# Performance work log

Measured on AMD Instinct MI355X. Metric: run time of the kernel, lower is better.

## Reference

```python
import jax, jax.numpy as jnp
import numpy as np

EMBED = 1024
HEADS = 16
HEAD_DIM = EMBED // HEADS
FF = 4 * EMBED
B, S = 2, 2048


def setup_inputs() -> dict:
    key = jax.random.key(0)
    ks = jax.random.split(key, 16)
    sd = 0.02
    inp = {
        "x": jax.random.normal(ks[0], (B, S, EMBED), dtype=jnp.float32),
        "Wq": jax.random.normal(ks[1], (EMBED, EMBED), dtype=jnp.float32) * sd,
        "bq": jnp.zeros((EMBED,), jnp.float32),
        "Wk": jax.random.normal(ks[2], (EMBED, EMBED), dtype=jnp.float32) * sd,
        "bk": jnp.zeros((EMBED,), jnp.float32),
        "Wv": jax.random.normal(ks[3], (EMBED, EMBED), dtype=jnp.float32) * sd,
        "bv": jnp.zeros((EMBED,), jnp.float32),
        "Wo": jax.random.normal(ks[4], (EMBED, EMBED), dtype=jnp.float32) * sd,
        "W1": jax.random.normal(ks[5], (EMBED, FF), dtype=jnp.float32) * sd,
        "b1": jnp.zeros((FF,), jnp.float32),
        "W2": jax.random.normal(ks[6], (FF, EMBED), dtype=jnp.float32) * sd,
        "b2": jnp.zeros((EMBED,), jnp.float32),
        "g1": jnp.ones((EMBED,), jnp.float32),
        "be1": jnp.zeros((EMBED,), jnp.float32),
        "g2": jnp.ones((EMBED,), jnp.float32),
        "be2": jnp.zeros((EMBED,), jnp.float32),
    }
    return inp


def _layernorm(x, g, b, eps=1e-5):
    mu = jnp.mean(x, axis=-1, keepdims=True)
    var = jnp.mean(jnp.square(x - mu), axis=-1, keepdims=True)
    return (x - mu) * jax.lax.rsqrt(var + eps) * g + b


def _attn(x, Wq, bq, Wk, bk, Wv, bv, Wo):
    b, s, d = x.shape
    q = (x @ Wq + bq).reshape(b, s, HEADS, HEAD_DIM)
    k = (x @ Wk + bk).reshape(b, s, HEADS, HEAD_DIM)
    v = (x @ Wv + bv).reshape(b, s, HEADS, HEAD_DIM)
    # NOTE: original scales by sqrt(embed_dim), NOT sqrt(head_dim)
    logits = jnp.einsum('bqhd,bkhd->bhqk', q, k) / jnp.sqrt(jnp.float32(d))
    mask = jnp.tril(jnp.ones((s, s), dtype=bool))
    logits = jnp.where(mask, logits, -jnp.inf)
    w = jax.nn.softmax(logits, axis=-1)
    z = jnp.einsum('bhqk,bkhd->bqhd', w, v).reshape(b, s, d)
    return z @ Wo


def reference(x, Wq, bq, Wk, bk, Wv, bv, Wo, W1, b1, W2, b2, g1, be1, g2, be2):
    h = x + _attn(_layernorm(x, g1, be1), Wq, bq, Wk, bk, Wv, bv, Wo)
    m = _layernorm(h, g2, be2)
    m = jax.nn.gelu(m @ W1 + b1, approximate=False) @ W2 + b2
    return h + m
```

## Files before the change

kernel.cpp:

```cpp
#include <hip/hip_runtime.h>
#include <cstdint>
#include <cstddef>
#include <math.h>

#define EMBED 1024
#define SEQ   2048
#define NROWS 4096
#define NHEADS 16

typedef __bf16 bf16x8 __attribute__((ext_vector_type(8)));
typedef float f32x4 __attribute__((ext_vector_type(4)));
typedef unsigned short us8 __attribute__((ext_vector_type(8)));
typedef unsigned short us4 __attribute__((ext_vector_type(4)));

__device__ __forceinline__ unsigned short f2bf(float f) {
  union { float f; unsigned u; } v; v.f = f;
  unsigned r = v.u + 0x7fffu + ((v.u >> 16) & 1u);
  return (unsigned short)(r >> 16);
}
__device__ __forceinline__ float bf2f(unsigned short u) {
  union { unsigned u; float f; } v; v.u = (unsigned)u << 16; return v.f;
}

__device__ __forceinline__ bf16x8 as_bf(us8 u) { return __builtin_bit_cast(bf16x8, u); }

__device__ __forceinline__ void gload_lds16(const unsigned short* g, unsigned short* l) {
  __builtin_amdgcn_global_load_lds((const __attribute__((address_space(1))) void*)g,
                                   (__attribute__((address_space(3))) void*)l, 16, 0, 0);
}

__global__ __launch_bounds__(256) void transpose_to_bf16(
    const float* __restrict__ in, unsigned short* __restrict__ out, int K, int N) {
  __shared__ float tile[32][33];
  const int tx = threadIdx.x & 31, ty = threadIdx.x >> 5;
  const int n0 = blockIdx.x * 32, k0 = blockIdx.y * 32;
#pragma unroll
  for (int i = 0; i < 4; i++) {
    int k = ty + i * 8;
    tile[k][tx] = in[(size_t)(k0 + k) * N + n0 + tx];
  }
  __syncthreads();
#pragma unroll
  for (int i = 0; i < 4; i++) {
    int n = ty + i * 8;
    out[(size_t)(n0 + n) * K + k0 + tx] = f2bf(tile[tx][n]);
  }
}

__global__ __launch_bounds__(256) void layernorm_bf16(
    const float* __restrict__ x, const float* __restrict__ g,
    const float* __restrict__ be, unsigned short* __restrict__ out) {
  const int wave = threadIdx.x >> 6, lane = threadIdx.x & 63;
  const int row = blockIdx.x * 4 + wave;
  const float* xr = x + (size_t)row * EMBED;
  float4 v[4];
  float s = 0.f, sq = 0.f;
#pragma unroll
  for (int c = 0; c < 4; c++) {
    v[c] = *(const float4*)&xr[c * 256 + lane * 4];
    s  += v[c].x + v[c].y + v[c].z + v[c].w;
    sq += v[c].x * v[c].x + v[c].y * v[c].y + v[c].z * v[c].z + v[c].w * v[c].w;
  }
#pragma unroll
  for (int m = 1; m < 64; m <<= 1) {
    s  += __shfl_xor(s, m, 64);
    sq += __shfl_xor(sq, m, 64);
  }
  const float mean = s * (1.f / 1024.f);
  const float var  = sq * (1.f / 1024.f) - mean * mean;
  const float rstd = rsqrtf(var + 1e-5f);
#pragma unroll
  for (int c = 0; c < 4; c++) {
    const int idx = c * 256 + lane * 4;
    us4 o;
    o[0] = f2bf((v[c].x - mean) * rstd * g[idx + 0] + be[idx + 0]);
    o[1] = f2bf((v[c].y - mean) * rstd * g[idx + 1] + be[idx + 1]);
    o[2] = f2bf((v[c].z - mean) * rstd * g[idx + 2] + be[idx + 2]);
    o[3] = f2bf((v[c].w - mean) * rstd * g[idx + 3] + be[idx + 3]);
    *(us4*)&out[(size_t)row * EMBED + idx] = o;
  }
}

enum { MODE_QKV = 0, MODE_WO = 1, MODE_FF1 = 2, MODE_FF2 = 3, MODE_PART = 4 };

template <int MODE>
__global__ __launch_bounds__(256) void gemm_bf16(
    const unsigned short* __restrict__ A,
    const unsigned short* __restrict__ Bt0,
    const unsigned short* __restrict__ Bt1,
    const unsigned short* __restrict__ Bt2,
    const float* __restrict__ bias0,
    const float* __restrict__ bias1,
    const float* __restrict__ bias2,
    const float* __restrict__ res,
    void* __restrict__ out0, void* __restrict__ out1,
    void* __restrict__ out2, void* __restrict__ out3,
    int M, int N, int K) {
  const unsigned short* Bt = Bt0;
  const float* bias = bias0;
  void* outv = out0;
  int zidx = 0;
  if constexpr (MODE == MODE_QKV) {
    zidx = blockIdx.z;
    if (zidx == 1)      { Bt = Bt1; bias = bias1; outv = out1; }
    else if (zidx == 2) { Bt = Bt2; bias = bias2; outv = out2; }
  }
  if constexpr (MODE == MODE_PART) {
    zidx = blockIdx.z;
    outv = (zidx == 0) ? out0 : (zidx == 1) ? out1 : (zidx == 2) ? out2 : out3;
  }
  const int Ksub = (MODE == MODE_PART) ? 1024 : K;
  const int koff = (MODE == MODE_PART) ? zidx * 1024 : 0;

  __shared__ unsigned short As[128 * 32];
  __shared__ unsigned short Bs[128 * 32];
  const int tid = threadIdx.x;
  const int wave = tid >> 6, lane = tid & 63;
  const int quad = lane >> 4, l15 = lane & 15;
  const int wr = (wave >> 1) * 64, wc = (wave & 1) * 64;
  const int rowA0 = blockIdx.y * 128, colB0 = blockIdx.x * 128;

  const int srow = tid >> 2;
  const int scol = (tid & 3) * 8;
  const unsigned short* gA = A  + (size_t)(rowA0 + srow) * K + koff + scol;
  const unsigned short* gB = Bt + (size_t)(colB0 + srow) * K + koff + scol;
  unsigned short* lA  = &As[tid * 8];
  unsigned short* lA2 = &As[2048 + tid * 8];
  unsigned short* lB  = &Bs[tid * 8];
  unsigned short* lB2 = &Bs[2048 + tid * 8];
  const size_t half = (size_t)64 * K;

  f32x4 acc[4][4];
#pragma unroll
  for (int i = 0; i < 4; i++)
#pragma unroll
    for (int j = 0; j < 4; j++) acc[i][j] = f32x4{0.f, 0.f, 0.f, 0.f};

  for (int k0 = 0; k0 < Ksub; k0 += 32) {
    gload_lds16(gA + k0, lA);
    gload_lds16(gA + half + k0, lA2);
    gload_lds16(gB + k0, lB);
    gload_lds16(gB + half + k0, lB2);
    __syncthreads();
    bf16x8 af[4], bfr[4];
#pragma unroll
    for (int mi = 0; mi < 4; mi++)
      af[mi] = as_bf(*(const us8*)&As[(wr + mi * 16 + l15) * 32 + quad * 8]);
#pragma unroll
    for (int ni = 0; ni < 4; ni++)
      bfr[ni] = as_bf(*(const us8*)&Bs[(wc + ni * 16 + l15) * 32 + quad * 8]);
#pragma unroll
    for (int mi = 0; mi < 4; mi++)
#pragma unroll
      for (int ni = 0; ni < 4; ni++)
        acc[mi][ni] = __builtin_amdgcn_mfma_f32_16x16x32_bf16(af[mi], bfr[ni], acc[mi][ni], 0, 0, 0);
    __syncthreads();
  }

#pragma unroll
  for (int ni = 0; ni < 4; ni++) {
    const int col = colB0 + wc + ni * 16 + l15;
    float bv = 0.f;
    if constexpr (MODE == MODE_QKV || MODE == MODE_FF1 || MODE == MODE_FF2) bv = bias[col];
#pragma unroll
    for (int mi = 0; mi < 4; mi++) {
      const int row0 = rowA0 + wr + mi * 16 + quad * 4;
      if constexpr (MODE == MODE_QKV) {
        unsigned short* o = (unsigned short*)outv;
        if (zidx == 2) {
          us4 pk;
#pragma unroll
          for (int r = 0; r < 4; r++) pk[r] = f2bf(acc[mi][ni][r] + bv);
          const int bb = row0 >> 11;
          const int sr = row0 & 2047;
          *(us4*)&o[((size_t)(bb * 1024 + col)) * SEQ + sr] = pk;
        } else {
#pragma unroll
          for (int r = 0; r < 4; r++)
            o[(size_t)(row0 + r) * N + col] = f2bf(acc[mi][ni][r] + bv);
        }
      } else if constexpr (MODE == MODE_FF1) {
        unsigned short* o = (unsigned short*)outv;
#pragma unroll
        for (int r = 0; r < 4; r++) {
          float v = acc[mi][ni][r] + bv;
          v = 0.5f * v * (1.f + erff(v * 0.7071067811865476f));
          o[(size_t)(row0 + r) * N + col] = f2bf(v);
        }
      } else if constexpr (MODE == MODE_PART) {
        unsigned short* o = (unsigned short*)outv;
#pragma unroll
        for (int r = 0; r < 4; r++)
          o[(size_t)(row0 + r) * N + col] = f2bf(acc[mi][ni][r]);
      } else {
        float* o = (float*)outv;
#pragma unroll
        for (int r = 0; r < 4; r++) {
          float v = acc[mi][ni][r] + bv + res[(size_t)(row0 + r) * N + col];
          o[(size_t)(row0 + r) * N + col] = v;
        }
      }
    }
  }
}

__global__ __launch_bounds__(256) void ff2_reduce(
    const float* __restrict__ hb, const float* __restrict__ b2,
    const unsigned short* __restrict__ p0, const unsigned short* __restrict__ p1,
    const unsigned short* __restrict__ p2, const unsigned short* __restrict__ p3,
    float* __restrict__ out) {
  const size_t i = ((size_t)blockIdx.x * 256 + threadIdx.x) * 4;
  const int col = (int)(i & (EMBED - 1));
  const float4 h = *(const float4*)&hb[i];
  const float4 bb = *(const float4*)&b2[col];
  const us4 a = *(const us4*)&p0[i];
  const us4 b = *(const us4*)&p1[i];
  const us4 c = *(const us4*)&p2[i];
  const us4 d = *(const us4*)&p3[i];
  float4 o;
  o.x = h.x + bb.x + bf2f(a[0]) + bf2f(b[0]) + bf2f(c[0]) + bf2f(d[0]);
  o.y = h.y + bb.y + bf2f(a[1]) + bf2f(b[1]) + bf2f(c[1]) + bf2f(d[1]);
  o.z = h.z + bb.z + bf2f(a[2]) + bf2f(b[2]) + bf2f(c[2]) + bf2f(d[2]);
  o.w = h.w + bb.w + bf2f(a[3]) + bf2f(b[3]) + bf2f(c[3]) + bf2f(d[3]);
  *(float4*)&out[i] = o;
}

__global__ __launch_bounds__(256) void attn_kernel(
    const unsigned short* __restrict__ Q,
    const unsigned short* __restrict__ Kb,
    const unsigned short* __restrict__ Vt,
    unsigned short* __restrict__ Z) {
  __shared__ unsigned short Ksh[2][64][32];
  __shared__ unsigned short Vsh[2][64][32];
  __shared__ unsigned short Pt[4][16][72];
  __shared__ float Ot[4][64][17];

  const int wave = threadIdx.x >> 6, lane = threadIdx.x & 63;
  const int quad = lane >> 4, l15 = lane & 15;
  const int bh = blockIdx.x, b = bh >> 4, h = bh & 15;
  const int qt = blockIdx.y;
  const int q0 = qt * 128 + wave * 32;
  const float cscale = 1.4426950408889634f / 32.f;

  bf16x8 qf[2][2];
#pragma unroll
  for (int c = 0; c < 2; c++)
#pragma unroll
    for (int kf = 0; kf < 2; kf++)
      qf[c][kf] = as_bf(*(const us8*)&Q[(size_t)(b * SEQ + q0 + c * 16 + l15) * EMBED +
                                        h * 64 + kf * 32 + quad * 8]);

  f32x4 accO[2][4];
#pragma unroll
  for (int c = 0; c < 2; c++)
#pragma unroll
    for (int dt = 0; dt < 4; dt++) accO[c][dt] = f32x4{0.f, 0.f, 0.f, 0.f};
  float mrun[2] = {-INFINITY, -INFINITY};
  float lrun[2] = {0.f, 0.f};

  const int ls_row = lane >> 2;
  const int ls_c16 = lane & 3;
  const int nkt = 2 * qt + 2;

  for (int kt = 0; kt < nkt; kt++) {
    const int kbase = kt * 64;
    const int krow = wave * 16 + ls_row;
#pragma unroll
    for (int kf = 0; kf < 2; kf++) {
      const unsigned short* g =
          &Kb[(size_t)(b * SEQ + kbase + krow) * EMBED + h * 64 + kf * 32 + ls_c16 * 8];
      gload_lds16(g, &Ksh[kf][wave * 16][0] + lane * 8);
    }
#pragma unroll
    for (int kk = 0; kk < 2; kk++) {
      const unsigned short* g =
          &Vt[(size_t)(b * 1024 + h * 64 + krow) * SEQ + kbase + kk * 32 + ls_c16 * 8];
      gload_lds16(g, &Vsh[kk][wave * 16][0] + lane * 8);
    }
    __syncthreads();

#pragma unroll
    for (int c = 0; c < 2; c++) {
      const int qc = q0 + c * 16;
      if (kbase > qc + 15) continue;
      f32x4 sf[4];
#pragma unroll
      for (int nt = 0; nt < 4; nt++) {
        f32x4 z4 = f32x4{0.f, 0.f, 0.f, 0.f};
#pragma unroll
        for (int kf = 0; kf < 2; kf++) {
          const bf16x8 ka = as_bf(*(const us8*)&Ksh[kf][nt * 16 + l15][quad * 8]);
          z4 = __builtin_amdgcn_mfma_f32_16x16x32_bf16(ka, qf[c][kf], z4, 0, 0, 0);
        }
        sf[nt] = z4 * cscale;
      }
      if (kbase + 63 > qc) {
        const int q = qc + l15;
#pragma unroll
        for (int nt = 0; nt < 4; nt++) {
          const int key0 = kbase + nt * 16 + quad * 4;
#pragma unroll
          for (int r = 0; r < 4; r++)
            if (key0 + r > q) sf[nt][r] = -INFINITY;
        }
      }
      float mx = sf[0][0];
#pragma unroll
      for (int nt = 0; nt < 4; nt++)
#pragma unroll
        for (int r = 0; r < 4; r++) mx = fmaxf(mx, sf[nt][r]);
      mx = fmaxf(mx, __shfl_xor(mx, 16, 64));
      mx = fmaxf(mx, __shfl_xor(mx, 32, 64));
      const float mnew = fmaxf(mrun[c], mx);
      const float alpha = exp2f(mrun[c] - mnew);
      mrun[c] = mnew;
      float rs = 0.f;
#pragma unroll
      for (int nt = 0; nt < 4; nt++) {
        us4 pk;
#pragma unroll
        for (int r = 0; r < 4; r++) {
          const float p = exp2f(sf[nt][r] - mnew);
          rs += p;
          pk[r] = f2bf(p);
        }
        *(us4*)&Pt[wave][l15][nt * 16 + quad * 4] = pk;
      }
      rs += __shfl_xor(rs, 16, 64);
      rs += __shfl_xor(rs, 32, 64);
      lrun[c] = lrun[c] * alpha + rs;
#pragma unroll
      for (int dt = 0; dt < 4; dt++) accO[c][dt] = accO[c][dt] * alpha;
      bf16x8 pf[2];
#pragma unroll
      for (int kk = 0; kk < 2; kk++)
        pf[kk] = as_bf(*(const us8*)&Pt[wave][l15][kk * 32 + quad * 8]);
#pragma unroll
      for (int dt = 0; dt < 4; dt++)
#pragma unroll
        for (int kk = 0; kk < 2; kk++) {
          const bf16x8 va = as_bf(*(const us8*)&Vsh[kk][dt * 16 + l15][quad * 8]);
          accO[c][dt] = __builtin_amdgcn_mfma_f32_16x16x32_bf16(va, pf[kk], accO[c][dt], 0, 0, 0);
        }
    }
    __syncthreads();
  }

#pragma unroll
  for (int c = 0; c < 2; c++) {
    const float inv = 1.f / lrun[c];
#pragma unroll
    for (int dt = 0; dt < 4; dt++)
#pragma unroll
      for (int r = 0; r < 4; r++)
        Ot[wave][dt * 16 + quad * 4 + r][l15] = accO[c][dt][r] * inv;
    const int lq = lane >> 2, dbase = (lane & 3) * 16;
    us8 o0, o1;
#pragma unroll
    for (int i = 0; i < 8; i++) o0[i] = f2bf(Ot[wave][dbase + i][lq]);
#pragma unroll
    for (int i = 0; i < 8; i++) o1[i] = f2bf(Ot[wave][dbase + 8 + i][lq]);
    unsigned short* zp = Z + (size_t)(b * SEQ + q0 + c * 16 + lq) * EMBED + h * 64 + dbase;
    *(us8*)zp = o0;
    *(us8*)(zp + 8) = o1;
  }
}

extern "C" void kernel_launch(void* const* d_in, const int* in_sizes, int n_in,
                              void* d_out, int out_size, void* d_ws, size_t ws_size,
                              hipStream_t stream) {
  const float* x   = (const float*)d_in[0];
  const float* Wq  = (const float*)d_in[1];
  const float* bq  = (const float*)d_in[2];
  const float* Wk  = (const float*)d_in[3];
  const float* bk  = (const float*)d_in[4];
  const float* Wv  = (const float*)d_in[5];
  const float* bv  = (const float*)d_in[6];
  const float* Wo  = (const float*)d_in[7];
  const float* W1  = (const float*)d_in[8];
  const float* b1  = (const float*)d_in[9];
  const float* W2  = (const float*)d_in[10];
  const float* b2  = (const float*)d_in[11];
  const float* g1  = (const float*)d_in[12];
  const float* be1 = (const float*)d_in[13];
  const float* g2  = (const float*)d_in[14];
  const float* be2 = (const float*)d_in[15];
  float* out = (float*)d_out;

  char* ws = (char*)d_ws;
  const size_t MB = 1024 * 1024;
  unsigned short* wqT = (unsigned short*)(ws + 0 * MB);
  unsigned short* wkT = (unsigned short*)(ws + 2 * MB);
  unsigned short* wvT = (unsigned short*)(ws + 4 * MB);
  unsigned short* woT = (unsigned short*)(ws + 6 * MB);
  unsigned short* w1T = (unsigned short*)(ws + 8 * MB);
  unsigned short* w2T = (unsigned short*)(ws + 16 * MB);
  unsigned short* ln1 = (unsigned short*)(ws + 24 * MB);
  unsigned short* qb  = (unsigned short*)(ws + 32 * MB);
  unsigned short* kb2 = (unsigned short*)(ws + 40 * MB);
  unsigned short* vT  = (unsigned short*)(ws + 48 * MB);
  unsigned short* zb  = (unsigned short*)(ws + 24 * MB);
  float*          hb  = (float*)         (ws + 32 * MB);
  unsigned short* ln2 = (unsigned short*)(ws + 48 * MB);
  unsigned short* m1  = (unsigned short*)(ws + 56 * MB);
  unsigned short* p0  = (unsigned short*)(ws + 0 * MB);
  unsigned short* p1  = (unsigned short*)(ws + 8 * MB);
  unsigned short* p2  = (unsigned short*)(ws + 24 * MB);
  unsigned short* p3  = (unsigned short*)(ws + 48 * MB);
  (void)in_sizes; (void)n_in; (void)out_size; (void)ws_size;

  transpose_to_bf16<<<dim3(32, 32), 256, 0, stream>>>(Wq, wqT, 1024, 1024);
  transpose_to_bf16<<<dim3(32, 32), 256, 0, stream>>>(Wk, wkT, 1024, 1024);
  transpose_to_bf16<<<dim3(32, 32), 256, 0, stream>>>(Wv, wvT, 1024, 1024);
  transpose_to_bf16<<<dim3(32, 32), 256, 0, stream>>>(Wo, woT, 1024, 1024);
  transpose_to_bf16<<<dim3(128, 32), 256, 0, stream>>>(W1, w1T, 1024, 4096);
  transpose_to_bf16<<<dim3(32, 128), 256, 0, stream>>>(W2, w2T, 4096, 1024);

  layernorm_bf16<<<NROWS / 4, 256, 0, stream>>>(x, g1, be1, ln1);

  gemm_bf16<MODE_QKV><<<dim3(8, 32, 3), 256, 0, stream>>>(
      ln1, wqT, wkT, wvT, bq, bk, bv, nullptr, qb, kb2, vT, nullptr,
      NROWS, 1024, 1024);

  attn_kernel<<<dim3(32, 16), 256, 0, stream>>>(qb, kb2, vT, zb);

  gemm_bf16<MODE_WO><<<dim3(8, 32), 256, 0, stream>>>(
      zb, woT, nullptr, nullptr, nullptr, nullptr, nullptr, x,
      hb, nullptr, nullptr, nullptr, NROWS, 1024, 1024);

  layernorm_bf16<<<NROWS / 4, 256, 0, stream>>>(hb, g2, be2, ln2);

  gemm_bf16<MODE_FF1><<<dim3(32, 32), 256, 0, stream>>>(
      ln2, w1T, nullptr, nullptr, b1, nullptr, nullptr, nullptr,
      m1, nullptr, nullptr, nullptr, NROWS, 4096, 1024);

  gemm_bf16<MODE_PART><<<dim3(8, 32, 4), 256, 0, stream>>>(
      m1, w2T, nullptr, nullptr, nullptr, nullptr, nullptr, nullptr,
      p0, p1, p2, p3, NROWS, 1024, 4096);

  ff2_reduce<<<NROWS * EMBED / (256 * 4), 256, 0, stream>>>(
      hb, b2, p0, p1, p2, p3, out);
}
```

Measured before the change: 439.0 us.

## Balance causal attention blocks, split-K the Wo GEMM, fuse residual into LN2

The attention kernel now gives each block two 64-row query tiles, j and 31-j, so every block does about the same causal work. K/V tiles are staged into padded LDS through registers instead of direct global-to-LDS loads. The Wo projection becomes a two-way split-K partial GEMM, and a new fused kernel sums x with the two bf16 partials, writes h and computes LayerNorm2. The split doubles the Wo grid for occupancy but rounds the partials to bf16, which loses some precision in the residual.

Result: faster. 416.0 us (-5.2%).

```diff
diff --git a/kernel.cpp b/kernel.cpp
--- a/kernel.cpp
+++ b/kernel.cpp
@@ -78,6 +78,51 @@
     o[2] = f2bf((v[c].z - mean) * rstd * g[idx + 2] + be[idx + 2]);
     o[3] = f2bf((v[c].w - mean) * rstd * g[idx + 3] + be[idx + 3]);
     *(us4*)&out[(size_t)row * EMBED + idx] = o;
+  }
+}
+
+__global__ __launch_bounds__(256) void ln2_fused(
+    const float* __restrict__ x,
+    const unsigned short* __restrict__ pw0,
+    const unsigned short* __restrict__ pw1,
+    const float* __restrict__ g, const float* __restrict__ be,
+    float* __restrict__ hb, unsigned short* __restrict__ out) {
+  const int wave = threadIdx.x >> 6, lane = threadIdx.x & 63;
+  const int row = blockIdx.x * 4 + wave;
+  const size_t rb = (size_t)row * EMBED;
+  float4 v[4];
+  float s = 0.f, sq = 0.f;
+#pragma unroll
+  for (int c = 0; c < 4; c++) {
+    const int idx = c * 256 + lane * 4;
+    const float4 xv = *(const float4*)&x[rb + idx];
+    const us4 a = *(const us4*)&pw0[rb + idx];
+    const us4 d = *(const us4*)&pw1[rb + idx];
+    v[c].x = xv.x + bf2f(a[0]) + bf2f(d[0]);
+    v[c].y = xv.y + bf2f(a[1]) + bf2f(d[1]);
+    v[c].z = xv.z + bf2f(a[2]) + bf2f(d[2]);
+    v[c].w = xv.w + bf2f(a[3]) + bf2f(d[3]);
+    *(float4*)&hb[rb + idx] = v[c];
+    s  += v[c].x + v[c].y + v[c].z + v[c].w;
+    sq += v[c].x * v[c].x + v[c].y * v[c].y + v[c].z * v[c].z + v[c].w * v[c].w;
+  }
+#pragma unroll
+  for (int m = 1; m < 64; m <<= 1) {
+    s  += __shfl_xor(s, m, 64);
+    sq += __shfl_xor(sq, m, 64);
+  }
+  const float mean = s * (1.f / 1024.f);
+  const float var  = sq * (1.f / 1024.f) - mean * mean;
+  const float rstd = rsqrtf(var + 1e-5f);
+#pragma unroll
+  for (int c = 0; c < 4; c++) {
+    const int idx = c * 256 + lane * 4;
+    us4 o;
+    o[0] = f2bf((v[c].x - mean) * rstd * g[idx + 0] + be[idx + 0]);
+    o[1] = f2bf((v[c].y - mean) * rstd * g[idx + 1] + be[idx + 1]);
+    o[2] = f2bf((v[c].z - mean) * rstd * g[idx + 2] + be[idx + 2]);
+    o[3] = f2bf((v[c].w - mean) * rstd * g[idx + 3] + be[idx + 3]);
+    *(us4*)&out[rb + idx] = o;
   }
 }
 
@@ -109,8 +154,8 @@
     zidx = blockIdx.z;
     outv = (zidx == 0) ? out0 : (zidx == 1) ? out1 : (zidx == 2) ? out2 : out3;
   }
-  const int Ksub = (MODE == MODE_PART) ? 1024 : K;
-  const int koff = (MODE == MODE_PART) ? zidx * 1024 : 0;
+  const int Ksub = (MODE == MODE_PART) ? K / (int)gridDim.z : K;
+  const int koff = (MODE == MODE_PART) ? zidx * Ksub : 0;
 
   __shared__ unsigned short As[128 * 32];
   __shared__ unsigned short Bs[128 * 32];
@@ -230,71 +275,65 @@
     const unsigned short* __restrict__ Kb,
     const unsigned short* __restrict__ Vt,
     unsigned short* __restrict__ Z) {
-  __shared__ unsigned short Ksh[2][64][32];
-  __shared__ unsigned short Vsh[2][64][32];
+  __shared__ unsigned short Ksh[64][72];
+  __shared__ unsigned short Vsh[64][72];
   __shared__ unsigned short Pt[4][16][72];
   __shared__ float Ot[4][64][17];
 
-  const int wave = threadIdx.x >> 6, lane = threadIdx.x & 63;
+  const int tid = threadIdx.x;
+  const int wave = tid >> 6, lane = tid & 63;
   const int quad = lane >> 4, l15 = lane & 15;
   const int bh = blockIdx.x, b = bh >> 4, h = bh & 15;
-  const int qt = blockIdx.y;
-  const int q0 = qt * 128 + wave * 32;
   const float cscale = 1.4426950408889634f / 32.f;
 
-  bf16x8 qf[2][2];
-#pragma unroll
-  for (int c = 0; c < 2; c++)
+  const int srow = tid >> 2;
+  const int sc = (tid & 3) * 8;
+  const unsigned short* Kbase = Kb + (size_t)(b * SEQ) * EMBED + h * 64;
+  const unsigned short* Vbase = Vt + (size_t)(b * 1024 + h * 64) * SEQ;
+
+#pragma unroll
+  for (int ph = 0; ph < 2; ph++) {
+    const int j = ph ? 31 - (int)blockIdx.y : (int)blockIdx.y;
+    const int qc = j * 64 + wave * 16;
+
+    bf16x8 qf[2];
 #pragma unroll
     for (int kf = 0; kf < 2; kf++)
-      qf[c][kf] = as_bf(*(const us8*)&Q[(size_t)(b * SEQ + q0 + c * 16 + l15) * EMBED +
-                                        h * 64 + kf * 32 + quad * 8]);
-
-  f32x4 accO[2][4];
-#pragma unroll
-  for (int c = 0; c < 2; c++)
-#pragma unroll
-    for (int dt = 0; dt < 4; dt++) accO[c][dt] = f32x4{0.f, 0.f, 0.f, 0.f};
-  float mrun[2] = {-INFINITY, -INFINITY};
-  float lrun[2] = {0.f, 0.f};
-
-  const int ls_row = lane >> 2;
-  const int ls_c16 = lane & 3;
-  const int nkt = 2 * qt + 2;
-
-  for (int kt = 0; kt < nkt; kt++) {
-    const int kbase = kt * 64;
-    const int krow = wave * 16 + ls_row;
-#pragma unroll
-    for (int kf = 0; kf < 2; kf++) {
-      const unsigned short* g =
-          &Kb[(size_t)(b * SEQ + kbase + krow) * EMBED + h * 64 + kf * 32 + ls_c16 * 8];
-      gload_lds16(g, &Ksh[kf][wave * 16][0] + lane * 8);
-    }
-#pragma unroll
-    for (int kk = 0; kk < 2; kk++) {
-      const unsigned short* g =
-          &Vt[(size_t)(b * 1024 + h * 64 + krow) * SEQ + kbase + kk * 32 + ls_c16 * 8];
-      gload_lds16(g, &Vsh[kk][wave * 16][0] + lane * 8);
-    }
-    __syncthreads();
-
-#pragma unroll
-    for (int c = 0; c < 2; c++) {
-      const int qc = q0 + c * 16;
-      if (kbase > qc + 15) continue;
+      qf[kf] = as_bf(*(const us8*)&Q[(size_t)(b * SEQ + qc + l15) * EMBED +
+                                     h * 64 + kf * 32 + quad * 8]);
+
+    f32x4 accO[4];
+#pragma unroll
+    for (int dt = 0; dt < 4; dt++) accO[dt] = f32x4{0.f, 0.f, 0.f, 0.f};
+    float mrun = -INFINITY, lrun = 0.f;
+
+    for (int kt = 0; kt <= j; kt++) {
+      const int kbase = kt * 64;
+      const unsigned short* kg = Kbase + (size_t)(kbase + srow) * EMBED + sc;
+      const unsigned short* vg = Vbase + (size_t)srow * SEQ + kbase + sc;
+      const us8 k0 = *(const us8*)kg;
+      const us8 k1 = *(const us8*)(kg + 32);
+      const us8 v0 = *(const us8*)vg;
+      const us8 v1 = *(const us8*)(vg + 32);
+      __syncthreads();
+      *(us8*)&Ksh[srow][sc]      = k0;
+      *(us8*)&Ksh[srow][32 + sc] = k1;
+      *(us8*)&Vsh[srow][sc]      = v0;
+      *(us8*)&Vsh[srow][32 + sc] = v1;
+      __syncthreads();
+
       f32x4 sf[4];
 #pragma unroll
       for (int nt = 0; nt < 4; nt++) {
         f32x4 z4 = f32x4{0.f, 0.f, 0.f, 0.f};
 #pragma unroll
         for (int kf = 0; kf < 2; kf++) {
-          const bf16x8 ka = as_bf(*(const us8*)&Ksh[kf][nt * 16 + l15][quad * 8]);
-          z4 = __builtin_amdgcn_mfma_f32_16x16x32_bf16(ka, qf[c][kf], z4, 0, 0, 0);
+          const bf16x8 ka = as_bf(*(const us8*)&Ksh[nt * 16 + l15][kf * 32 + quad * 8]);
+          z4 = __builtin_amdgcn_mfma_f32_16x16x32_bf16(ka, qf[kf], z4, 0, 0, 0);
         }
         sf[nt] = z4 * cscale;
       }
-      if (kbase + 63 > qc) {
+      if (kt == j) {
         const int q = qc + l15;
 #pragma unroll
         for (int nt = 0; nt < 4; nt++) {
@@ -311,9 +350,9 @@
         for (int r = 0; r < 4; r++) mx = fmaxf(mx, sf[nt][r]);
       mx = fmaxf(mx, __shfl_xor(mx, 16, 64));
       mx = fmaxf(mx, __shfl_xor(mx, 32, 64));
-      const float mnew = fmaxf(mrun[c], mx);
-      const float alpha = exp2f(mrun[c] - mnew);
-      mrun[c] = mnew;
+      const float mnew = fmaxf(mrun, mx);
+      const float alpha = exp2f(mrun - mnew);
+      mrun = mnew;
       float rs = 0.f;
 #pragma unroll
       for (int nt = 0; nt < 4; nt++) {
@@ -328,9 +367,9 @@
       }
       rs += __shfl_xor(rs, 16, 64);
       rs += __shfl_xor(rs, 32, 64);
-      lrun[c] = lrun[c] * alpha + rs;
-#pragma unroll
-      for (int dt = 0; dt < 4; dt++) accO[c][dt] = accO[c][dt] * alpha;
+      lrun = lrun * alpha + rs;
+#pragma unroll
+      for (int dt = 0; dt < 4; dt++) accO[dt] = accO[dt] * alpha;
       bf16x8 pf[2];
 #pragma unroll
       for (int kk = 0; kk < 2; kk++)
@@ -339,28 +378,24 @@
       for (int dt = 0; dt < 4; dt++)
 #pragma unroll
         for (int kk = 0; kk < 2; kk++) {
-          const bf16x8 va = as_bf(*(const us8*)&Vsh[kk][dt * 16 + l15][quad * 8]);
-          accO[c][dt] = __builtin_amdgcn_mfma_f32_16x16x32_bf16(va, pf[kk], accO[c][dt], 0, 0, 0);
+          const bf16x8 va = as_bf(*(const us8*)&Vsh[dt * 16 + l15][kk * 32 + quad * 8]);
+          accO[dt] = __builtin_amdgcn_mfma_f32_16x16x32_bf16(va, pf[kk], accO[dt], 0, 0, 0);
         }
     }
-    __syncthreads();
-  }
-
-#pragma unroll
-  for (int c = 0; c < 2; c++) {
-    const float inv = 1.f / lrun[c];
+
+    const float inv = 1.f / lrun;
 #pragma unroll
     for (int dt = 0; dt < 4; dt++)
 #pragma unroll
       for (int r = 0; r < 4; r++)
-        Ot[wave][dt * 16 + quad * 4 + r][l15] = accO[c][dt][r] * inv;
+        Ot[wave][dt * 16 + quad * 4 + r][l15] = accO[dt][r] * inv;
     const int lq = lane >> 2, dbase = (lane & 3) * 16;
     us8 o0, o1;
 #pragma unroll
     for (int i = 0; i < 8; i++) o0[i] = f2bf(Ot[wave][dbase + i][lq]);
 #pragma unroll
     for (int i = 0; i < 8; i++) o1[i] = f2bf(Ot[wave][dbase + 8 + i][lq]);
-    unsigned short* zp = Z + (size_t)(b * SEQ + q0 + c * 16 + lq) * EMBED + h * 64 + dbase;
+    unsigned short* zp = Z + (size_t)(b * SEQ + qc + lq) * EMBED + h * 64 + dbase;
     *(us8*)zp = o0;
     *(us8*)(zp + 8) = o1;
   }
@@ -396,17 +431,19 @@
   unsigned short* w1T = (unsigned short*)(ws + 8 * MB);
   unsigned short* w2T = (unsigned short*)(ws + 16 * MB);
   unsigned short* ln1 = (unsigned short*)(ws + 24 * MB);
+  unsigned short* zb  = (unsigned short*)(ws + 24 * MB);
+  unsigned short* ln2 = (unsigned short*)(ws + 24 * MB);
+  unsigned short* p2  = (unsigned short*)(ws + 24 * MB);
   unsigned short* qb  = (unsigned short*)(ws + 32 * MB);
   unsigned short* kb2 = (unsigned short*)(ws + 40 * MB);
+  float*          hb  = (float*)         (ws + 32 * MB);
   unsigned short* vT  = (unsigned short*)(ws + 48 * MB);
-  unsigned short* zb  = (unsigned short*)(ws + 24 * MB);
-  float*          hb  = (float*)         (ws + 32 * MB);
-  unsigned short* ln2 = (unsigned short*)(ws + 48 * MB);
+  unsigned short* pw0 = (unsigned short*)(ws + 48 * MB);
+  unsigned short* p3  = (unsigned short*)(ws + 48 * MB);
+  unsigned short* pw1 = (unsigned short*)(ws + 56 * MB);
   unsigned short* m1  = (unsigned short*)(ws + 56 * MB);
   unsigned short* p0  = (unsigned short*)(ws + 0 * MB);
   unsigned short* p1  = (unsigned short*)(ws + 8 * MB);
-  unsigned short* p2  = (unsigned short*)(ws + 24 * MB);
-  unsigned short* p3  = (unsigned short*)(ws + 48 * MB);
   (void)in_sizes; (void)n_in; (void)out_size; (void)ws_size;
 
   transpose_to_bf16<<<dim3(32, 32), 256, 0, stream>>>(Wq, wqT, 1024, 1024);
@@ -424,11 +461,11 @@
 
   attn_kernel<<<dim3(32, 16), 256, 0, stream>>>(qb, kb2, vT, zb);
 
-  gemm_bf16<MODE_WO><<<dim3(8, 32), 256, 0, stream>>>(
-      zb, woT, nullptr, nullptr, nullptr, nullptr, nullptr, x,
-      hb, nullptr, nullptr, nullptr, NROWS, 1024, 1024);
-
-  layernorm_bf16<<<NROWS / 4, 256, 0, stream>>>(hb, g2, be2, ln2);
+  gemm_bf16<MODE_PART><<<dim3(8, 32, 2), 256, 0, stream>>>(
+      zb, woT, nullptr, nullptr, nullptr, nullptr, nullptr, nullptr,
+      pw0, pw1, nullptr, nullptr, NROWS, 1024, 1024);
+
+  ln2_fused<<<NROWS / 4, 256, 0, stream>>>(x, pw0, pw1, g2, be2, hb, ln2);
 
   gemm_bf16<MODE_FF1><<<dim3(32, 32), 256, 0, stream>>>(
       ln2, w1T, nullptr, nullptr, b1, nullptr, nullptr, nullptr,
```
